# Performance work log

Measured on AMD Instinct MI355X. Metric: run time of the kernel, lower is better.

## Reference

```python
import jax, jax.numpy as jnp
import numpy as np

N_NODES = 50000
N_EDGES = 800000
IN_DIM = 128
HID_DIM = 256
OUT_DIM = 5
BATCH = 50000  # batch_size in module; view(batch_size, 5)


def _sage_conv(x, src, dst, Wl, bl, Wr):
    # PyG SAGEConv (aggr='mean', root_weight=True, normalize=False):
    #   out = lin_l(mean_{j in N(i)} x_j) + lin_r(x_i)
    msgs = x[src]                                            # [E, d]
    agg = jax.ops.segment_sum(msgs, dst, num_segments=N_NODES)
    cnt = jax.ops.segment_sum(jnp.ones((src.shape[0],), x.dtype), dst,
                              num_segments=N_NODES)          # [N]
    mean = agg / jnp.maximum(cnt, 1.0)[:, None]              # 0 for isolated nodes
    return mean @ Wl.T + bl + x @ Wr.T


def setup_inputs() -> dict:
    key = jax.random.key(0)
    ks = jax.random.split(key, 8)
    x = jax.random.normal(ks[0], (N_NODES, IN_DIM), dtype=jnp.float32)
    edge_index = jax.random.randint(ks[1], (2, N_EDGES), 0, N_NODES, dtype=jnp.int64)
    s1 = 1.0 / np.sqrt(IN_DIM)
    s2 = 1.0 / np.sqrt(HID_DIM)
    W1l = jax.random.uniform(ks[2], (HID_DIM, IN_DIM), jnp.float32, -s1, s1)
    b1l = jax.random.uniform(ks[3], (HID_DIM,), jnp.float32, -s1, s1)
    W1r = jax.random.uniform(ks[4], (HID_DIM, IN_DIM), jnp.float32, -s1, s1)
    W2l = jax.random.uniform(ks[5], (OUT_DIM, HID_DIM), jnp.float32, -s2, s2)
    b2l = jax.random.uniform(ks[6], (OUT_DIM,), jnp.float32, -s2, s2)
    W2r = jax.random.uniform(ks[7], (OUT_DIM, HID_DIM), jnp.float32, -s2, s2)
    return {"x": x, "edge_index": edge_index,
            "W1l": W1l, "b1l": b1l, "W1r": W1r,
            "W2l": W2l, "b2l": b2l, "W2r": W2r}


def reference(x, edge_index, W1l, b1l, W1r, W2l, b2l, W2r):
    src, dst = edge_index[0], edge_index[1]
    h = jax.nn.relu(_sage_conv(x, src, dst, W1l, b1l, W1r))   # [N, hidden]
    h = jax.nn.relu(_sage_conv(h, src, dst, W2l, b2l, W2r))   # [N, out]
    return h.reshape(BATCH, 5)
```

## Files before the change

### kernel.cpp

```cpp
#include <hip/hip_runtime.h>

static constexpr int NN = 50000;
static constexpr int NE = 800000;
static constexpr int D0 = 128;
static constexpr int D1 = 256;
static constexpr int D2 = 5;

static constexpr int XB = (NN * 32 + 255) / 256;
static constexpr int WB = (D1 * 64) / 256;
static constexpr int PB = 4;

static constexpr int BSZ   = 512;
static constexpr int NBUK  = (NN + BSZ - 1) / BSZ;
static constexpr int CAP   = 9216;
static constexpr int CB    = 400;
static constexpr int CHUNK = 2000;

using short8  = __attribute__((ext_vector_type(8))) short;
using floatx4 = __attribute__((ext_vector_type(4))) float;

__device__ __forceinline__ unsigned short f2b(float f) {
  union { float f; unsigned u; } v; v.f = f;
  unsigned r = v.u + 0x7fffu + ((v.u >> 16) & 1u);
  return (unsigned short)(r >> 16);
}
__device__ __forceinline__ float b2f(unsigned short s) {
  union { unsigned u; float f; } v; v.u = ((unsigned)s) << 16;
  return v.f;
}

__global__ __launch_bounds__(256) void k_prepA(
    const float* __restrict__ x, unsigned short* __restrict__ ab,
    const float* __restrict__ W1l, const float* __restrict__ W1r,
    unsigned short* __restrict__ wb, const float* __restrict__ W2l,
    const float* __restrict__ W2r, unsigned short* __restrict__ w2b,
    const int* __restrict__ src, const int* __restrict__ dst,
    int* __restrict__ gcur, uint2* __restrict__ slab) {
  __shared__ int hist[128], bstart[128], gbase[128], hcur[128], sscan[128];
  __shared__ uint2 pairs[CHUNK];
  const int b = blockIdx.x, t = threadIdx.x;
  if (b < XB) {
    int idx = b * 256 + t;
    if (idx < NN * 32) {
      int node = idx >> 5, cg = idx & 31;
      float4 v = *(const float4*)(x + (size_t)node * D0 + cg * 4);
      ushort4 o;
      o.x = f2b(v.x); o.y = f2b(v.y); o.z = f2b(v.z); o.w = f2b(v.w);
      *(ushort4*)(ab + (size_t)node * 256 + 128 + cg * 4) = o;
    }
    return;
  }
  if (b < XB + WB) {
    int idx = (b - XB) * 256 + t;
    int c = idx >> 6, k = (idx & 63) * 4;
    const float* srcp = (k < 128) ? (W1l + (size_t)c * 128 + k)
                                  : (W1r + (size_t)c * 128 + (k - 128));
    float4 v = *(const float4*)srcp;
    ushort4 o;
    o.x = f2b(v.x); o.y = f2b(v.y); o.z = f2b(v.z); o.w = f2b(v.w);
    *(ushort4*)(wb + (size_t)c * 256 + k) = o;
    return;
  }
  if (b < XB + WB + PB) {
    int idx = (b - XB - WB) * 256 + t;
    int n = idx >> 6, k = (idx & 63) * 4;
    float4 v = {0.f, 0.f, 0.f, 0.f};
    if (n < 5) v = *(const float4*)(W2l + (size_t)n * D1 + k);
    else if (n < 10) v = *(const float4*)(W2r + (size_t)(n - 5) * D1 + k);
    ushort4 o;
    o.x = f2b(v.x); o.y = f2b(v.y); o.z = f2b(v.z); o.w = f2b(v.w);
    *(ushort4*)(w2b + (size_t)n * 256 + k) = o;
    return;
  }
  const int ba = b - (XB + WB + PB);
  const int e0 = ba * CHUNK;
  if (t < 128) hist[t] = 0;
  __syncthreads();
  for (int j = t; j < CHUNK; j += 256)
    atomicAdd(&hist[dst[e0 + j] >> 9], 1);
  __syncthreads();
  if (t < 128) sscan[t] = hist[t];
  __syncthreads();
  for (int dd = 1; dd < 128; dd <<= 1) {
    int u = (t >= dd && t < 128) ? sscan[t - dd] : 0;
    __syncthreads();
    if (t < 128) sscan[t] += u;
    __syncthreads();
  }
  if (t < 128) {
    bstart[t] = sscan[t] - hist[t];
    gbase[t] = (t < NBUK && hist[t] > 0) ? atomicAdd(&gcur[t], hist[t]) : 0;
    hcur[t] = 0;
  }
  __syncthreads();
  for (int j = t; j < CHUNK; j += 256) {
    const int s = src[e0 + j], d = dst[e0 + j];
    const int bk = d >> 9;
    const int pos = bstart[bk] + atomicAdd(&hcur[bk], 1);
    pairs[pos] = make_uint2((unsigned)s, (unsigned)d);
  }
  __syncthreads();
  for (int j = t; j < CHUNK; j += 256) {
    const uint2 pr = pairs[j];
    const int bk = (int)pr.y >> 9;
    slab[(size_t)bk * CAP + gbase[bk] + (j - bstart[bk])] = pr;
  }
}

__global__ __launch_bounds__(512) void k_bucketBC(
    const uint2* __restrict__ slab, const int* __restrict__ gcur,
    int* __restrict__ cur, float* __restrict__ inv,
    int* __restrict__ esort) {
  __shared__ int cnt[BSZ], s[BSZ], lcur[BSZ], g[128];
  const int b = blockIdx.x, t = threadIdx.x;
  const int n0 = b << 9;
  cnt[t] = 0;
  if (t < 128) g[t] = (t < NBUK) ? gcur[t] : 0;
  __syncthreads();
  for (int dd = 1; dd < 128; dd <<= 1) {
    int u = (t >= dd && t < 128) ? g[t - dd] : 0;
    __syncthreads();
    if (t < 128) g[t] += u;
    __syncthreads();
  }
  const int bbase = (b == 0) ? 0 : g[b - 1];
  const int cntE = gcur[b];
  const uint2* sp = slab + (size_t)b * CAP;
  for (int j = t; j < cntE; j += 512)
    atomicAdd(&cnt[(int)sp[j].y - n0], 1);
  __syncthreads();
  s[t] = cnt[t];
  __syncthreads();
  for (int dd = 1; dd < BSZ; dd <<= 1) {
    int u = (t >= dd) ? s[t - dd] : 0;
    __syncthreads();
    s[t] += u;
    __syncthreads();
  }
  const int start = bbase + (s[t] - cnt[t]);
  const int node = n0 + t;
  if (node < NN) {
    cur[node] = start;
    inv[node] = 1.0f / (float)max(cnt[t], 1);
  }
  lcur[t] = start;
  if (b == NBUK - 1 && t == 0) cur[NN] = NE;
  __syncthreads();
  for (int j = t; j < cntE; j += 512) {
    const uint2 pr = sp[j];
    const int p = atomicAdd(&lcur[(int)pr.y - n0], 1);
    esort[p] = (int)pr.x;
  }
}

__global__ __launch_bounds__(256) void k_agg1(
    unsigned short* __restrict__ ab, const int* __restrict__ esort,
    const int* __restrict__ cur, const float* __restrict__ inv) {
  const int i = (blockIdx.x * 256 + threadIdx.x) >> 6;
  const int lane = threadIdx.x & 63;
  if (i >= NN) return;
  int e = cur[i];
  const int end = cur[i + 1];
  float a0 = 0.f, b0 = 0.f, a1 = 0.f, b1 = 0.f;
  float a2 = 0.f, b2 = 0.f, a3 = 0.f, b3 = 0.f;
  const unsigned short* xb = ab + 128 + lane * 2;
  while (e < end && (e & 3)) {
    const unsigned v = *(const unsigned*)(xb + (size_t)esort[e] * 256);
    a0 += b2f((unsigned short)v); b0 += b2f((unsigned short)(v >> 16));
    ++e;
  }
  for (; e + 7 < end; e += 8) {
    const int4 s0 = *(const int4*)(esort + e);
    const int4 s1 = *(const int4*)(esort + e + 4);
    const unsigned v0 = *(const unsigned*)(xb + (size_t)s0.x * 256);
    const unsigned v1 = *(const unsigned*)(xb + (size_t)s0.y * 256);
    const unsigned v2 = *(const unsigned*)(xb + (size_t)s0.z * 256);
    const unsigned v3 = *(const unsigned*)(xb + (size_t)s0.w * 256);
    const unsigned v4 = *(const unsigned*)(xb + (size_t)s1.x * 256);
    const unsigned v5 = *(const unsigned*)(xb + (size_t)s1.y * 256);
    const unsigned v6 = *(const unsigned*)(xb + (size_t)s1.z * 256);
    const unsigned v7 = *(const unsigned*)(xb + (size_t)s1.w * 256);
    a0 += b2f((unsigned short)v0); b0 += b2f((unsigned short)(v0 >> 16));
    a1 += b2f((unsigned short)v1); b1 += b2f((unsigned short)(v1 >> 16));
    a2 += b2f((unsigned short)v2); b2 += b2f((unsigned short)(v2 >> 16));
    a3 += b2f((unsigned short)v3); b3 += b2f((unsigned short)(v3 >> 16));
    a0 += b2f((unsigned short)v4); b0 += b2f((unsigned short)(v4 >> 16));
    a1 += b2f((unsigned short)v5); b1 += b2f((unsigned short)(v5 >> 16));
    a2 += b2f((unsigned short)v6); b2 += b2f((unsigned short)(v6 >> 16));
    a3 += b2f((unsigned short)v7); b3 += b2f((unsigned short)(v7 >> 16));
  }
  if (e + 3 < end) {
    const int4 s0 = *(const int4*)(esort + e);
    const unsigned v0 = *(const unsigned*)(xb + (size_t)s0.x * 256);
    const unsigned v1 = *(const unsigned*)(xb + (size_t)s0.y * 256);
    const unsigned v2 = *(const unsigned*)(xb + (size_t)s0.z * 256);
    const unsigned v3 = *(const unsigned*)(xb + (size_t)s0.w * 256);
    a0 += b2f((unsigned short)v0); b0 += b2f((unsigned short)(v0 >> 16));
    a1 += b2f((unsigned short)v1); b1 += b2f((unsigned short)(v1 >> 16));
    a2 += b2f((unsigned short)v2); b2 += b2f((unsigned short)(v2 >> 16));
    a3 += b2f((unsigned short)v3); b3 += b2f((unsigned short)(v3 >> 16));
    e += 4;
  }
  for (; e < end; ++e) {
    const unsigned v = *(const unsigned*)(xb + (size_t)esort[e] * 256);
    a0 += b2f((unsigned short)v); b0 += b2f((unsigned short)(v >> 16));
  }
  const float sc = inv[i];
  const float sa = (a0 + a1) + (a2 + a3);
  const float sb = (b0 + b1) + (b2 + b3);
  const unsigned out =
      ((unsigned)f2b(sb * sc) << 16) | (unsigned)f2b(sa * sc);
  *(unsigned*)(ab + (size_t)i * 256 + lane * 2) = out;
}

__global__ __launch_bounds__(256) void k_gemm1f(
    const unsigned short* __restrict__ ab, const unsigned short* __restrict__ wb,
    const unsigned short* __restrict__ w2b, const float* __restrict__ b1l,
    float* __restrict__ tt, float* __restrict__ rp) {
  __shared__ short sAB[2 * 128 * 72];
  short* sA = sAB;
  short* sB = sAB + 128 * 72;
  const int tid = threadIdx.x;
  const int row0 = blockIdx.y * 128;
  const int hf = blockIdx.x;
  const int col0 = hf * 128;
  const int wave = tid >> 6, lane = tid & 63;
  const int quad = lane >> 4, m16 = lane & 15;
  const int wm = wave & 1, wn = wave >> 1;
  const int lr = tid >> 2;
  const int lk = (tid & 3) * 8;

  floatx4 acc[4][4];
#pragma unroll
  for (int a = 0; a < 4; ++a)
#pragma unroll
    for (int b = 0; b < 4; ++b) acc[a][b] = {0.f, 0.f, 0.f, 0.f};

  const int gr0 = row0 + lr, gr1 = row0 + lr + 64;
  const bool ok0 = gr0 < NN, ok1 = gr1 < NN;
  const unsigned short* aptr0 = ab + (size_t)gr0 * 256 + lk;
  const unsigned short* aptr1 = ab + (size_t)gr1 * 256 + lk;
  const unsigned short* bptr0 = wb + (size_t)(col0 + lr) * 256 + lk;
  const unsigned short* bptr1 = wb + (size_t)(col0 + lr + 64) * 256 + lk;
  short* sA0 = &sA[lr * 72 + lk];
  short* sA1 = &sA[(lr + 64) * 72 + lk];
  short* sB0 = &sB[lr * 72 + lk];
  short* sB1 = &sB[(lr + 64) * 72 + lk];
  const uint4 zz = make_uint4(0, 0, 0, 0);

  for (int kk = 0; kk < 256; kk += 64) {
    const uint4 a00 = ok0 ? *(const uint4*)(aptr0 + kk) : zz;
    const uint4 a01 = ok0 ? *(const uint4*)(aptr0 + kk + 32) : zz;
    const uint4 a10 = ok1 ? *(const uint4*)(aptr1 + kk) : zz;
    const uint4 a11 = ok1 ? *(const uint4*)(aptr1 + kk + 32) : zz;
    const uint4 b00 = *(const uint4*)(bptr0 + kk);
    const uint4 b01 = *(const uint4*)(bptr0 + kk + 32);
    const uint4 b10 = *(const uint4*)(bptr1 + kk);
    const uint4 b11 = *(const uint4*)(bptr1 + kk + 32);
    __syncthreads();
    *(uint4*)sA0 = a00;
    *(uint4*)(sA0 + 32) = a01;
    *(uint4*)sA1 = a10;
    *(uint4*)(sA1 + 32) = a11;
    *(uint4*)sB0 = b00;
    *(uint4*)(sB0 + 32) = b01;
    *(uint4*)sB1 = b10;
    *(uint4*)(sB1 + 32) = b11;
    __syncthreads();
#pragma unroll
    for (int ko = 0; ko < 64; ko += 32) {
      short8 af[4], bf[4];
#pragma unroll
      for (int mt = 0; mt < 4; ++mt)
        af[mt] =
            *(const short8*)&sA[(wm * 64 + mt * 16 + m16) * 72 + ko + quad * 8];
#pragma unroll
      for (int nt = 0; nt < 4; ++nt)
        bf[nt] =
            *(const short8*)&sB[(wn * 64 + nt * 16 + m16) * 72 + ko + quad * 8];
#pragma unroll
      for (int mt = 0; mt < 4; ++mt)
#pragma unroll
        for (int nt = 0; nt < 4; ++nt)
          acc[mt][nt] = __builtin_amdgcn_mfma_f32_16x16x32_bf16(
              af[mt], bf[nt], acc[mt][nt], 0, 0, 0);
    }
  }

  __syncthreads();
  short* sH = sAB;
#pragma unroll
  for (int nt = 0; nt < 4; ++nt) {
    const int cl = wn * 64 + nt * 16 + m16;
    const float bias = b1l[col0 + cl];
#pragma unroll
    for (int mt = 0; mt < 4; ++mt)
#pragma unroll
      for (int rg = 0; rg < 4; ++rg) {
        const int rl = wm * 64 + mt * 16 + quad * 4 + rg;
        sH[rl * 136 + cl] = (short)f2b(fmaxf(acc[mt][nt][rg] + bias, 0.f));
      }
  }
  __syncthreads();
  floatx4 c2[2] = {{0.f, 0.f, 0.f, 0.f}, {0.f, 0.f, 0.f, 0.f}};
#pragma unroll
  for (int kb = 0; kb < 4; ++kb) {
    const short8 bf2 =
        *(const short8*)&w2b[m16 * 256 + col0 + kb * 32 + quad * 8];
#pragma unroll
    for (int i = 0; i < 2; ++i) {
      const int mrow = (wave * 2 + i) * 16 + m16;
      const short8 af2 = *(const short8*)&sH[mrow * 136 + kb * 32 + quad * 8];
      c2[i] = __builtin_amdgcn_mfma_f32_16x16x32_bf16(af2, bf2, c2[i], 0, 0, 0);
    }
  }
#pragma unroll
  for (int i = 0; i < 2; ++i) {
    const int rbase = row0 + (wave * 2 + i) * 16 + quad * 4;
#pragma unroll
    for (int rg = 0; rg < 4; ++rg) {
      const int row = rbase + rg;
      if (row < NN) {
        if (m16 < 5)
          tt[(size_t)row * 16 + hf * 8 + m16] = c2[i][rg];
        else if (m16 < 10)
          rp[(size_t)hf * ((size_t)NN * 8) + (size_t)row * 8 + (m16 - 5)] =
              c2[i][rg];
      }
    }
  }
}

__global__ __launch_bounds__(256) void k_layer2(
    const float* __restrict__ tt, const float* __restrict__ rp,
    const int* __restrict__ esort, const int* __restrict__ cur,
    const float* __restrict__ inv, const float* __restrict__ b2l,
    float* __restrict__ out) {
  const int node = blockIdx.x * 16 + (threadIdx.x >> 4);
  const int l = threadIdx.x & 15;
  if (node >= NN) return;
  const int beg = cur[node], end = cur[node + 1];
  float s0 = 0.f, s1 = 0.f, s2 = 0.f, s3 = 0.f, s4 = 0.f;
  for (int e = beg + l; e < end; e += 16) {
    const float* tp = tt + (size_t)esort[e] * 16;
    const float4 p0 = *(const float4*)tp;
    const float q0 = tp[4];
    const float4 p1 = *(const float4*)(tp + 8);
    const float q1 = tp[12];
    s0 += p0.x + p1.x;
    s1 += p0.y + p1.y;
    s2 += p0.z + p1.z;
    s3 += p0.w + p1.w;
    s4 += q0 + q1;
  }
#pragma unroll
  for (int m = 1; m < 16; m <<= 1) {
    s0 += __shfl_xor(s0, m, 64);
    s1 += __shfl_xor(s1, m, 64);
    s2 += __shfl_xor(s2, m, 64);
    s3 += __shfl_xor(s3, m, 64);
    s4 += __shfl_xor(s4, m, 64);
  }
  if (l == 0) {
    const float sc = inv[node];
    const float* r0 = rp + (size_t)node * 8;
    const float* r1 = rp + (size_t)NN * 8 + (size_t)node * 8;
    out[(size_t)node * D2 + 0] = fmaxf(s0 * sc + b2l[0] + r0[0] + r1[0], 0.f);
    out[(size_t)node * D2 + 1] = fmaxf(s1 * sc + b2l[1] + r0[1] + r1[1], 0.f);
    out[(size_t)node * D2 + 2] = fmaxf(s2 * sc + b2l[2] + r0[2] + r1[2], 0.f);
    out[(size_t)node * D2 + 3] = fmaxf(s3 * sc + b2l[3] + r0[3] + r1[3], 0.f);
    out[(size_t)node * D2 + 4] = fmaxf(s4 * sc + b2l[4] + r0[4] + r1[4], 0.f);
  }
}

extern "C" void kernel_launch(void* const* d_in, const int* in_sizes, int n_in,
                              void* d_out, int out_size, void* d_ws,
                              size_t ws_size, hipStream_t stream) {
  const float* x   = (const float*)d_in[0];
  const int*   ei  = (const int*)d_in[1];
  const int*   src = ei;
  const int*   dst = ei + NE;
  const float* W1l = (const float*)d_in[2];
  const float* b1l = (const float*)d_in[3];
  const float* W1r = (const float*)d_in[4];
  const float* W2l = (const float*)d_in[5];
  const float* b2l = (const float*)d_in[6];
  const float* W2r = (const float*)d_in[7];
  float* out = (float*)d_out;

  unsigned short* ab  = (unsigned short*)d_ws;
  unsigned short* wb  = ab + (size_t)NN * 256;
  unsigned short* w2b = wb + 256 * 256;
  float* tt   = (float*)(w2b + 16 * 256);
  float* rp   = tt + (size_t)NN * 16;
  uint2* slab = (uint2*)(rp + (size_t)NN * 16);
  int*   gcur = (int*)(slab + (size_t)NBUK * CAP);
  int*   cur  = gcur + 128;
  int*   esort = cur + NN + 1;
  float* inv  = (float*)(esort + NE);

  hipMemsetAsync(gcur, 0, 128 * sizeof(int), stream);

  k_prepA<<<XB + WB + PB + CB, 256, 0, stream>>>(x, ab, W1l, W1r, wb, W2l, W2r,
                                                 w2b, src, dst, gcur, slab);
  k_bucketBC<<<NBUK, 512, 0, stream>>>(slab, gcur, cur, inv, esort);
  k_agg1<<<(NN * 64 + 255) / 256, 256, 0, stream>>>(ab, esort, cur, inv);
  dim3 g1(2, (NN + 127) / 128);
  k_gemm1f<<<g1, 256, 0, stream>>>(ab, wb, w2b, b1l, tt, rp);
  k_layer2<<<(NN + 15) / 16, 256, 0, stream>>>(tt, rp, esort, cur, inv, b2l,
                                               out);
}
```

Baseline: 182.8 us.

## Fuse all stages into one persistent kernel with software grid barriers

Replaces five separate kernel launches with a single persistent kernel of 512 blocks that runs the conversion, bucketing, CSR build, aggregation, GEMM and layer-2 stages in sequence, separated by atomic-counter grid barriers. Destination buckets shrink from 512 to 256 nodes, with a matching smaller slab capacity. The aim is to remove launch gaps and tail effects between stages. In exchange each stage runs with a fixed grid, and the spin barriers depend on all 512 blocks being co-resident, which is not guaranteed under a normal launch and could deadlock or hit the guard timeout.

```diff
diff --git a/kernel.cpp b/kernel.cpp
--- a/kernel.cpp
+++ b/kernel.cpp
@@ -6,15 +6,18 @@
 static constexpr int D1 = 256;
 static constexpr int D2 = 5;
 
-static constexpr int XB = (NN * 32 + 255) / 256;
-static constexpr int WB = (D1 * 64) / 256;
-static constexpr int PB = 4;
-
-static constexpr int BSZ   = 512;
+static constexpr int NB  = 512;
+static constexpr int TPB = 256;
+
+static constexpr int BSZ   = 256;
 static constexpr int NBUK  = (NN + BSZ - 1) / BSZ;
-static constexpr int CAP   = 9216;
+static constexpr int CAP   = 4800;
 static constexpr int CB    = 400;
 static constexpr int CHUNK = 2000;
+
+static constexpr int NTILE = 2 * ((NN + 127) / 128);
+
+static constexpr int SMEM_BYTES = 36864;
 
 using short8  = __attribute__((ext_vector_type(8))) short;
 using floatx4 = __attribute__((ext_vector_type(4))) float;
@@ -29,347 +32,360 @@
   return v.f;
 }
 
-__global__ __launch_bounds__(256) void k_prepA(
-    const float* __restrict__ x, unsigned short* __restrict__ ab,
-    const float* __restrict__ W1l, const float* __restrict__ W1r,
-    unsigned short* __restrict__ wb, const float* __restrict__ W2l,
-    const float* __restrict__ W2r, unsigned short* __restrict__ w2b,
-    const int* __restrict__ src, const int* __restrict__ dst,
-    int* __restrict__ gcur, uint2* __restrict__ slab) {
-  __shared__ int hist[128], bstart[128], gbase[128], hcur[128], sscan[128];
-  __shared__ uint2 pairs[CHUNK];
-  const int b = blockIdx.x, t = threadIdx.x;
-  if (b < XB) {
-    int idx = b * 256 + t;
-    if (idx < NN * 32) {
-      int node = idx >> 5, cg = idx & 31;
-      float4 v = *(const float4*)(x + (size_t)node * D0 + cg * 4);
-      ushort4 o;
-      o.x = f2b(v.x); o.y = f2b(v.y); o.z = f2b(v.z); o.w = f2b(v.w);
-      *(ushort4*)(ab + (size_t)node * 256 + 128 + cg * 4) = o;
-    }
-    return;
-  }
-  if (b < XB + WB) {
-    int idx = (b - XB) * 256 + t;
-    int c = idx >> 6, k = (idx & 63) * 4;
+__device__ __forceinline__ void gbar(int* ctr) {
+  __syncthreads();
+  if (threadIdx.x == 0) {
+    __threadfence();
+    atomicAdd(ctr, 1);
+    long guard = 0;
+    while (__hip_atomic_load(ctr, __ATOMIC_ACQUIRE, __HIP_MEMORY_SCOPE_AGENT) <
+               NB &&
+           ++guard < 100000000L) {
+    }
+  }
+  __syncthreads();
+}
+
+__global__ __launch_bounds__(256, 2) void k_all(
+    const float* __restrict__ x, const int* __restrict__ src,
+    const int* __restrict__ dst, const float* __restrict__ W1l,
+    const float* __restrict__ b1l, const float* __restrict__ W1r,
+    const float* __restrict__ W2l, const float* __restrict__ b2l,
+    const float* __restrict__ W2r, unsigned short* __restrict__ ab,
+    unsigned short* __restrict__ wb, unsigned short* __restrict__ w2b,
+    float* __restrict__ tt, float* __restrict__ rp, uint2* __restrict__ slab,
+    int* __restrict__ gcur, int* __restrict__ cur, float* __restrict__ inv,
+    int* __restrict__ esort, int* __restrict__ ctr, float* __restrict__ out) {
+  __shared__ __align__(16) char smem[SMEM_BYTES];
+  const int t = threadIdx.x;
+  const int bx = blockIdx.x;
+  const int gid = bx * TPB + t;
+
+  for (int idx = gid; idx < NN * 32; idx += NB * TPB) {
+    const int node = idx >> 5, cg4 = idx & 31;
+    const float4 v = *(const float4*)(x + (size_t)node * D0 + cg4 * 4);
+    ushort4 o;
+    o.x = f2b(v.x); o.y = f2b(v.y); o.z = f2b(v.z); o.w = f2b(v.w);
+    *(ushort4*)(ab + (size_t)node * 256 + 128 + cg4 * 4) = o;
+  }
+  for (int idx = gid; idx < 256 * 64; idx += NB * TPB) {
+    const int c = idx >> 6, k = (idx & 63) * 4;
     const float* srcp = (k < 128) ? (W1l + (size_t)c * 128 + k)
                                   : (W1r + (size_t)c * 128 + (k - 128));
-    float4 v = *(const float4*)srcp;
+    const float4 v = *(const float4*)srcp;
     ushort4 o;
     o.x = f2b(v.x); o.y = f2b(v.y); o.z = f2b(v.z); o.w = f2b(v.w);
     *(ushort4*)(wb + (size_t)c * 256 + k) = o;
-    return;
-  }
-  if (b < XB + WB + PB) {
-    int idx = (b - XB - WB) * 256 + t;
-    int n = idx >> 6, k = (idx & 63) * 4;
+  }
+  if (gid < 1024) {
+    const int n = gid >> 6, k = (gid & 63) * 4;
     float4 v = {0.f, 0.f, 0.f, 0.f};
     if (n < 5) v = *(const float4*)(W2l + (size_t)n * D1 + k);
     else if (n < 10) v = *(const float4*)(W2r + (size_t)(n - 5) * D1 + k);
     ushort4 o;
     o.x = f2b(v.x); o.y = f2b(v.y); o.z = f2b(v.z); o.w = f2b(v.w);
     *(ushort4*)(w2b + (size_t)n * 256 + k) = o;
-    return;
-  }
-  const int ba = b - (XB + WB + PB);
-  const int e0 = ba * CHUNK;
-  if (t < 128) hist[t] = 0;
-  __syncthreads();
-  for (int j = t; j < CHUNK; j += 256)
-    atomicAdd(&hist[dst[e0 + j] >> 9], 1);
-  __syncthreads();
-  if (t < 128) sscan[t] = hist[t];
-  __syncthreads();
-  for (int dd = 1; dd < 128; dd <<= 1) {
-    int u = (t >= dd && t < 128) ? sscan[t - dd] : 0;
-    __syncthreads();
-    if (t < 128) sscan[t] += u;
-    __syncthreads();
-  }
-  if (t < 128) {
-    bstart[t] = sscan[t] - hist[t];
+  }
+
+  if (bx < CB) {
+    int* hist = (int*)smem;
+    int* ss = hist + 256;
+    int* bstart = ss + 256;
+    int* hcur = bstart + 256;
+    int* gbase = hcur + 256;
+    uint2* pairs = (uint2*)(gbase + 256);
+    const int e0 = bx * CHUNK;
+    hist[t] = 0;
+    __syncthreads();
+    for (int j = t; j < CHUNK; j += TPB) atomicAdd(&hist[dst[e0 + j] >> 8], 1);
+    __syncthreads();
+    ss[t] = hist[t];
+    __syncthreads();
+    for (int dd = 1; dd < 256; dd <<= 1) {
+      const int u = (t >= dd) ? ss[t - dd] : 0;
+      __syncthreads();
+      ss[t] += u;
+      __syncthreads();
+    }
+    bstart[t] = ss[t] - hist[t];
+    hcur[t] = 0;
     gbase[t] = (t < NBUK && hist[t] > 0) ? atomicAdd(&gcur[t], hist[t]) : 0;
-    hcur[t] = 0;
-  }
-  __syncthreads();
-  for (int j = t; j < CHUNK; j += 256) {
-    const int s = src[e0 + j], d = dst[e0 + j];
-    const int bk = d >> 9;
-    const int pos = bstart[bk] + atomicAdd(&hcur[bk], 1);
-    pairs[pos] = make_uint2((unsigned)s, (unsigned)d);
-  }
-  __syncthreads();
-  for (int j = t; j < CHUNK; j += 256) {
-    const uint2 pr = pairs[j];
-    const int bk = (int)pr.y >> 9;
-    slab[(size_t)bk * CAP + gbase[bk] + (j - bstart[bk])] = pr;
-  }
-}
-
-__global__ __launch_bounds__(512) void k_bucketBC(
-    const uint2* __restrict__ slab, const int* __restrict__ gcur,
-    int* __restrict__ cur, float* __restrict__ inv,
-    int* __restrict__ esort) {
-  __shared__ int cnt[BSZ], s[BSZ], lcur[BSZ], g[128];
-  const int b = blockIdx.x, t = threadIdx.x;
-  const int n0 = b << 9;
-  cnt[t] = 0;
-  if (t < 128) g[t] = (t < NBUK) ? gcur[t] : 0;
-  __syncthreads();
-  for (int dd = 1; dd < 128; dd <<= 1) {
-    int u = (t >= dd && t < 128) ? g[t - dd] : 0;
-    __syncthreads();
-    if (t < 128) g[t] += u;
-    __syncthreads();
-  }
-  const int bbase = (b == 0) ? 0 : g[b - 1];
-  const int cntE = gcur[b];
-  const uint2* sp = slab + (size_t)b * CAP;
-  for (int j = t; j < cntE; j += 512)
-    atomicAdd(&cnt[(int)sp[j].y - n0], 1);
-  __syncthreads();
-  s[t] = cnt[t];
-  __syncthreads();
-  for (int dd = 1; dd < BSZ; dd <<= 1) {
-    int u = (t >= dd) ? s[t - dd] : 0;
-    __syncthreads();
-    s[t] += u;
-    __syncthreads();
-  }
-  const int start = bbase + (s[t] - cnt[t]);
-  const int node = n0 + t;
-  if (node < NN) {
-    cur[node] = start;
-    inv[node] = 1.0f / (float)max(cnt[t], 1);
-  }
-  lcur[t] = start;
-  if (b == NBUK - 1 && t == 0) cur[NN] = NE;
-  __syncthreads();
-  for (int j = t; j < cntE; j += 512) {
-    const uint2 pr = sp[j];
-    const int p = atomicAdd(&lcur[(int)pr.y - n0], 1);
-    esort[p] = (int)pr.x;
-  }
-}
-
-__global__ __launch_bounds__(256) void k_agg1(
-    unsigned short* __restrict__ ab, const int* __restrict__ esort,
-    const int* __restrict__ cur, const float* __restrict__ inv) {
-  const int i = (blockIdx.x * 256 + threadIdx.x) >> 6;
-  const int lane = threadIdx.x & 63;
-  if (i >= NN) return;
-  int e = cur[i];
-  const int end = cur[i + 1];
-  float a0 = 0.f, b0 = 0.f, a1 = 0.f, b1 = 0.f;
-  float a2 = 0.f, b2 = 0.f, a3 = 0.f, b3 = 0.f;
-  const unsigned short* xb = ab + 128 + lane * 2;
-  while (e < end && (e & 3)) {
-    const unsigned v = *(const unsigned*)(xb + (size_t)esort[e] * 256);
-    a0 += b2f((unsigned short)v); b0 += b2f((unsigned short)(v >> 16));
-    ++e;
-  }
-  for (; e + 7 < end; e += 8) {
-    const int4 s0 = *(const int4*)(esort + e);
-    const int4 s1 = *(const int4*)(esort + e + 4);
-    const unsigned v0 = *(const unsigned*)(xb + (size_t)s0.x * 256);
-    const unsigned v1 = *(const unsigned*)(xb + (size_t)s0.y * 256);
-    const unsigned v2 = *(const unsigned*)(xb + (size_t)s0.z * 256);
-    const unsigned v3 = *(const unsigned*)(xb + (size_t)s0.w * 256);
-    const unsigned v4 = *(const unsigned*)(xb + (size_t)s1.x * 256);
-    const unsigned v5 = *(const unsigned*)(xb + (size_t)s1.y * 256);
-    const unsigned v6 = *(const unsigned*)(xb + (size_t)s1.z * 256);
-    const unsigned v7 = *(const unsigned*)(xb + (size_t)s1.w * 256);
-    a0 += b2f((unsigned short)v0); b0 += b2f((unsigned short)(v0 >> 16));
-    a1 += b2f((unsigned short)v1); b1 += b2f((unsigned short)(v1 >> 16));
-    a2 += b2f((unsigned short)v2); b2 += b2f((unsigned short)(v2 >> 16));
-    a3 += b2f((unsigned short)v3); b3 += b2f((unsigned short)(v3 >> 16));
-    a0 += b2f((unsigned short)v4); b0 += b2f((unsigned short)(v4 >> 16));
-    a1 += b2f((unsigned short)v5); b1 += b2f((unsigned short)(v5 >> 16));
-    a2 += b2f((unsigned short)v6); b2 += b2f((unsigned short)(v6 >> 16));
-    a3 += b2f((unsigned short)v7); b3 += b2f((unsigned short)(v7 >> 16));
-  }
-  if (e + 3 < end) {
-    const int4 s0 = *(const int4*)(esort + e);
-    const unsigned v0 = *(const unsigned*)(xb + (size_t)s0.x * 256);
-    const unsigned v1 = *(const unsigned*)(xb + (size_t)s0.y * 256);
-    const unsigned v2 = *(const unsigned*)(xb + (size_t)s0.z * 256);
-    const unsigned v3 = *(const unsigned*)(xb + (size_t)s0.w * 256);
-    a0 += b2f((unsigned short)v0); b0 += b2f((unsigned short)(v0 >> 16));
-    a1 += b2f((unsigned short)v1); b1 += b2f((unsigned short)(v1 >> 16));
-    a2 += b2f((unsigned short)v2); b2 += b2f((unsigned short)(v2 >> 16));
-    a3 += b2f((unsigned short)v3); b3 += b2f((unsigned short)(v3 >> 16));
-    e += 4;
-  }
-  for (; e < end; ++e) {
-    const unsigned v = *(const unsigned*)(xb + (size_t)esort[e] * 256);
-    a0 += b2f((unsigned short)v); b0 += b2f((unsigned short)(v >> 16));
-  }
-  const float sc = inv[i];
-  const float sa = (a0 + a1) + (a2 + a3);
-  const float sb = (b0 + b1) + (b2 + b3);
-  const unsigned out =
-      ((unsigned)f2b(sb * sc) << 16) | (unsigned)f2b(sa * sc);
-  *(unsigned*)(ab + (size_t)i * 256 + lane * 2) = out;
-}
-
-__global__ __launch_bounds__(256) void k_gemm1f(
-    const unsigned short* __restrict__ ab, const unsigned short* __restrict__ wb,
-    const unsigned short* __restrict__ w2b, const float* __restrict__ b1l,
-    float* __restrict__ tt, float* __restrict__ rp) {
-  __shared__ short sAB[2 * 128 * 72];
-  short* sA = sAB;
-  short* sB = sAB + 128 * 72;
-  const int tid = threadIdx.x;
-  const int row0 = blockIdx.y * 128;
-  const int hf = blockIdx.x;
-  const int col0 = hf * 128;
-  const int wave = tid >> 6, lane = tid & 63;
-  const int quad = lane >> 4, m16 = lane & 15;
-  const int wm = wave & 1, wn = wave >> 1;
-  const int lr = tid >> 2;
-  const int lk = (tid & 3) * 8;
-
-  floatx4 acc[4][4];
-#pragma unroll
-  for (int a = 0; a < 4; ++a)
-#pragma unroll
-    for (int b = 0; b < 4; ++b) acc[a][b] = {0.f, 0.f, 0.f, 0.f};
-
-  const int gr0 = row0 + lr, gr1 = row0 + lr + 64;
-  const bool ok0 = gr0 < NN, ok1 = gr1 < NN;
-  const unsigned short* aptr0 = ab + (size_t)gr0 * 256 + lk;
-  const unsigned short* aptr1 = ab + (size_t)gr1 * 256 + lk;
-  const unsigned short* bptr0 = wb + (size_t)(col0 + lr) * 256 + lk;
-  const unsigned short* bptr1 = wb + (size_t)(col0 + lr + 64) * 256 + lk;
-  short* sA0 = &sA[lr * 72 + lk];
-  short* sA1 = &sA[(lr + 64) * 72 + lk];
-  short* sB0 = &sB[lr * 72 + lk];
-  short* sB1 = &sB[(lr + 64) * 72 + lk];
-  const uint4 zz = make_uint4(0, 0, 0, 0);
-
-  for (int kk = 0; kk < 256; kk += 64) {
-    const uint4 a00 = ok0 ? *(const uint4*)(aptr0 + kk) : zz;
-    const uint4 a01 = ok0 ? *(const uint4*)(aptr0 + kk + 32) : zz;
-    const uint4 a10 = ok1 ? *(const uint4*)(aptr1 + kk) : zz;
-    const uint4 a11 = ok1 ? *(const uint4*)(aptr1 + kk + 32) : zz;
-    const uint4 b00 = *(const uint4*)(bptr0 + kk);
-    const uint4 b01 = *(const uint4*)(bptr0 + kk + 32);
-    const uint4 b10 = *(const uint4*)(bptr1 + kk);
-    const uint4 b11 = *(const uint4*)(bptr1 + kk + 32);
-    __syncthreads();
-    *(uint4*)sA0 = a00;
-    *(uint4*)(sA0 + 32) = a01;
-    *(uint4*)sA1 = a10;
-    *(uint4*)(sA1 + 32) = a11;
-    *(uint4*)sB0 = b00;
-    *(uint4*)(sB0 + 32) = b01;
-    *(uint4*)sB1 = b10;
-    *(uint4*)(sB1 + 32) = b11;
-    __syncthreads();
-#pragma unroll
-    for (int ko = 0; ko < 64; ko += 32) {
-      short8 af[4], bf[4];
-#pragma unroll
-      for (int mt = 0; mt < 4; ++mt)
-        af[mt] =
-            *(const short8*)&sA[(wm * 64 + mt * 16 + m16) * 72 + ko + quad * 8];
-#pragma unroll
-      for (int nt = 0; nt < 4; ++nt)
-        bf[nt] =
-            *(const short8*)&sB[(wn * 64 + nt * 16 + m16) * 72 + ko + quad * 8];
-#pragma unroll
-      for (int mt = 0; mt < 4; ++mt)
-#pragma unroll
-        for (int nt = 0; nt < 4; ++nt)
-          acc[mt][nt] = __builtin_amdgcn_mfma_f32_16x16x32_bf16(
-              af[mt], bf[nt], acc[mt][nt], 0, 0, 0);
-    }
-  }
-
-  __syncthreads();
-  short* sH = sAB;
-#pragma unroll
-  for (int nt = 0; nt < 4; ++nt) {
-    const int cl = wn * 64 + nt * 16 + m16;
-    const float bias = b1l[col0 + cl];
-#pragma unroll
-    for (int mt = 0; mt < 4; ++mt)
-#pragma unroll
-      for (int rg = 0; rg < 4; ++rg) {
-        const int rl = wm * 64 + mt * 16 + quad * 4 + rg;
-        sH[rl * 136 + cl] = (short)f2b(fmaxf(acc[mt][nt][rg] + bias, 0.f));
-      }
-  }
-  __syncthreads();
-  floatx4 c2[2] = {{0.f, 0.f, 0.f, 0.f}, {0.f, 0.f, 0.f, 0.f}};
-#pragma unroll
-  for (int kb = 0; kb < 4; ++kb) {
-    const short8 bf2 =
-        *(const short8*)&w2b[m16 * 256 + col0 + kb * 32 + quad * 8];
-#pragma unroll
-    for (int i = 0; i < 2; ++i) {
-      const int mrow = (wave * 2 + i) * 16 + m16;
-      const short8 af2 = *(const short8*)&sH[mrow * 136 + kb * 32 + quad * 8];
-      c2[i] = __builtin_amdgcn_mfma_f32_16x16x32_bf16(af2, bf2, c2[i], 0, 0, 0);
-    }
-  }
-#pragma unroll
-  for (int i = 0; i < 2; ++i) {
-    const int rbase = row0 + (wave * 2 + i) * 16 + quad * 4;
-#pragma unroll
-    for (int rg = 0; rg < 4; ++rg) {
-      const int row = rbase + rg;
-      if (row < NN) {
-        if (m16 < 5)
-          tt[(size_t)row * 16 + hf * 8 + m16] = c2[i][rg];
-        else if (m16 < 10)
-          rp[(size_t)hf * ((size_t)NN * 8) + (size_t)row * 8 + (m16 - 5)] =
-              c2[i][rg];
-      }
-    }
-  }
-}
-
-__global__ __launch_bounds__(256) void k_layer2(
-    const float* __restrict__ tt, const float* __restrict__ rp,
-    const int* __restrict__ esort, const int* __restrict__ cur,
-    const float* __restrict__ inv, const float* __restrict__ b2l,
-    float* __restrict__ out) {
-  const int node = blockIdx.x * 16 + (threadIdx.x >> 4);
-  const int l = threadIdx.x & 15;
-  if (node >= NN) return;
-  const int beg = cur[node], end = cur[node + 1];
-  float s0 = 0.f, s1 = 0.f, s2 = 0.f, s3 = 0.f, s4 = 0.f;
-  for (int e = beg + l; e < end; e += 16) {
-    const float* tp = tt + (size_t)esort[e] * 16;
-    const float4 p0 = *(const float4*)tp;
-    const float q0 = tp[4];
-    const float4 p1 = *(const float4*)(tp + 8);
-    const float q1 = tp[12];
-    s0 += p0.x + p1.x;
-    s1 += p0.y + p1.y;
-    s2 += p0.z + p1.z;
-    s3 += p0.w + p1.w;
-    s4 += q0 + q1;
-  }
-#pragma unroll
-  for (int m = 1; m < 16; m <<= 1) {
-    s0 += __shfl_xor(s0, m, 64);
-    s1 += __shfl_xor(s1, m, 64);
-    s2 += __shfl_xor(s2, m, 64);
-    s3 += __shfl_xor(s3, m, 64);
-    s4 += __shfl_xor(s4, m, 64);
-  }
-  if (l == 0) {
-    const float sc = inv[node];
-    const float* r0 = rp + (size_t)node * 8;
-    const float* r1 = rp + (size_t)NN * 8 + (size_t)node * 8;
-    out[(size_t)node * D2 + 0] = fmaxf(s0 * sc + b2l[0] + r0[0] + r1[0], 0.f);
-    out[(size_t)node * D2 + 1] = fmaxf(s1 * sc + b2l[1] + r0[1] + r1[1], 0.f);
-    out[(size_t)node * D2 + 2] = fmaxf(s2 * sc + b2l[2] + r0[2] + r1[2], 0.f);
-    out[(size_t)node * D2 + 3] = fmaxf(s3 * sc + b2l[3] + r0[3] + r1[3], 0.f);
-    out[(size_t)node * D2 + 4] = fmaxf(s4 * sc + b2l[4] + r0[4] + r1[4], 0.f);
+    __syncthreads();
+    for (int j = t; j < CHUNK; j += TPB) {
+      const int s = src[e0 + j], d = dst[e0 + j];
+      const int bk = d >> 8;
+      const int pos = bstart[bk] + atomicAdd(&hcur[bk], 1);
+      pairs[pos] = make_uint2((unsigned)s, (unsigned)d);
+    }
+    __syncthreads();
+    for (int j = t; j < CHUNK; j += TPB) {
+      const uint2 pr = pairs[j];
+      const int bk = (int)pr.y >> 8;
+      slab[(size_t)bk * CAP + gbase[bk] + (j - bstart[bk])] = pr;
+    }
+  }
+  gbar(ctr + 0);
+
+  if (bx < NBUK) {
+    int* bs = (int*)smem;
+    int* cnt = bs + 256;
+    int* s = cnt + 256;
+    int* lcur = s + 256;
+    const int n0 = bx << 8;
+    bs[t] = (t < NBUK) ? gcur[t] : 0;
+    cnt[t] = 0;
+    __syncthreads();
+    for (int dd = 1; dd < 256; dd <<= 1) {
+      const int u = (t >= dd) ? bs[t - dd] : 0;
+      __syncthreads();
+      bs[t] += u;
+      __syncthreads();
+    }
+    const int bbase = (bx == 0) ? 0 : bs[bx - 1];
+    const int cntE = gcur[bx];
+    const uint2* sp = slab + (size_t)bx * CAP;
+    for (int j = t; j < cntE; j += TPB) atomicAdd(&cnt[(int)sp[j].y & 255], 1);
+    __syncthreads();
+    s[t] = cnt[t];
+    __syncthreads();
+    for (int dd = 1; dd < 256; dd <<= 1) {
+      const int u = (t >= dd) ? s[t - dd] : 0;
+      __syncthreads();
+      s[t] += u;
+      __syncthreads();
+    }
+    const int start = bbase + (s[t] - cnt[t]);
+    const int node = n0 + t;
+    if (node < NN) {
+      cur[node] = start;
+      inv[node] = 1.0f / (float)max(cnt[t], 1);
+    }
+    lcur[t] = start;
+    if (bx == 0 && t == 0) cur[NN] = bs[NBUK - 1];
+    __syncthreads();
+    for (int j = t; j < cntE; j += TPB) {
+      const uint2 pr = sp[j];
+      const int p = atomicAdd(&lcur[(int)pr.y & 255], 1);
+      esort[p] = (int)pr.x;
+    }
+  }
+  gbar(ctr + 1);
+
+  {
+    const int lane = t & 63;
+    const unsigned short* xb = ab + 128 + lane * 2;
+    for (int i = gid >> 6; i < NN; i += (NB * TPB) >> 6) {
+      int e = cur[i];
+      const int end = cur[i + 1];
+      float a0 = 0.f, b0 = 0.f, a1 = 0.f, b1 = 0.f;
+      float a2 = 0.f, b2 = 0.f, a3 = 0.f, b3 = 0.f;
+      while (e < end && (e & 3)) {
+        const unsigned v = *(const unsigned*)(xb + (size_t)esort[e] * 256);
+        a0 += b2f((unsigned short)v); b0 += b2f((unsigned short)(v >> 16));
+        ++e;
+      }
+      for (; e + 7 < end; e += 8) {
+        const int4 s0 = *(const int4*)(esort + e);
+        const int4 s1 = *(const int4*)(esort + e + 4);
+        const unsigned v0 = *(const unsigned*)(xb + (size_t)s0.x * 256);
+        const unsigned v1 = *(const unsigned*)(xb + (size_t)s0.y * 256);
+        const unsigned v2 = *(const unsigned*)(xb + (size_t)s0.z * 256);
+        const unsigned v3 = *(const unsigned*)(xb + (size_t)s0.w * 256);
+        const unsigned v4 = *(const unsigned*)(xb + (size_t)s1.x * 256);
+        const unsigned v5 = *(const unsigned*)(xb + (size_t)s1.y * 256);
+        const unsigned v6 = *(const unsigned*)(xb + (size_t)s1.z * 256);
+        const unsigned v7 = *(const unsigned*)(xb + (size_t)s1.w * 256);
+        a0 += b2f((unsigned short)v0); b0 += b2f((unsigned short)(v0 >> 16));
+        a1 += b2f((unsigned short)v1); b1 += b2f((unsigned short)(v1 >> 16));
+        a2 += b2f((unsigned short)v2); b2 += b2f((unsigned short)(v2 >> 16));
+        a3 += b2f((unsigned short)v3); b3 += b2f((unsigned short)(v3 >> 16));
+        a0 += b2f((unsigned short)v4); b0 += b2f((unsigned short)(v4 >> 16));
+        a1 += b2f((unsigned short)v5); b1 += b2f((unsigned short)(v5 >> 16));
+        a2 += b2f((unsigned short)v6); b2 += b2f((unsigned short)(v6 >> 16));
+        a3 += b2f((unsigned short)v7); b3 += b2f((unsigned short)(v7 >> 16));
+      }
+      if (e + 3 < end) {
+        const int4 s0 = *(const int4*)(esort + e);
+        const unsigned v0 = *(const unsigned*)(xb + (size_t)s0.x * 256);
+        const unsigned v1 = *(const unsigned*)(xb + (size_t)s0.y * 256);
+        const unsigned v2 = *(const unsigned*)(xb + (size_t)s0.z * 256);
+        const unsigned v3 = *(const unsigned*)(xb + (size_t)s0.w * 256);
+        a0 += b2f((unsigned short)v0); b0 += b2f((unsigned short)(v0 >> 16));
+        a1 += b2f((unsigned short)v1); b1 += b2f((unsigned short)(v1 >> 16));
+        a2 += b2f((unsigned short)v2); b2 += b2f((unsigned short)(v2 >> 16));
+        a3 += b2f((unsigned short)v3); b3 += b2f((unsigned short)(v3 >> 16));
+        e += 4;
+      }
+      for (; e < end; ++e) {
+        const unsigned v = *(const unsigned*)(xb + (size_t)esort[e] * 256);
+        a0 += b2f((unsigned short)v); b0 += b2f((unsigned short)(v >> 16));
+      }
+      const float sc = inv[i];
+      const float sa = (a0 + a1) + (a2 + a3);
+      const float sb = (b0 + b1) + (b2 + b3);
+      const unsigned o =
+          ((unsigned)f2b(sb * sc) << 16) | (unsigned)f2b(sa * sc);
+      *(unsigned*)(ab + (size_t)i * 256 + lane * 2) = o;
+    }
+  }
+  gbar(ctr + 2);
+
+  {
+    short* sA = (short*)smem;
+    short* sB = sA + 128 * 72;
+    const int wave = t >> 6, lane = t & 63;
+    const int quad = lane >> 4, m16 = lane & 15;
+    const int wm = wave & 1, wn = wave >> 1;
+    const int lr = t >> 2;
+    const int lk = (t & 3) * 8;
+    const uint4 zz = make_uint4(0, 0, 0, 0);
+    for (int tile = bx; tile < NTILE; tile += NB) {
+      const int row0 = (tile >> 1) * 128;
+      const int hf = tile & 1;
+      const int col0 = hf * 128;
+      floatx4 acc[4][4];
+#pragma unroll
+      for (int a = 0; a < 4; ++a)
+#pragma unroll
+        for (int b = 0; b < 4; ++b) acc[a][b] = {0.f, 0.f, 0.f, 0.f};
+      const int gr0 = row0 + lr, gr1 = row0 + lr + 64;
+      const bool ok0 = gr0 < NN, ok1 = gr1 < NN;
+      const unsigned short* aptr0 = ab + (size_t)gr0 * 256 + lk;
+      const unsigned short* aptr1 = ab + (size_t)gr1 * 256 + lk;
+      const unsigned short* bptr0 = wb + (size_t)(col0 + lr) * 256 + lk;
+      const unsigned short* bptr1 = wb + (size_t)(col0 + lr + 64) * 256 + lk;
+      short* sA0 = &sA[lr * 72 + lk];
+      short* sA1 = &sA[(lr + 64) * 72 + lk];
+      short* sB0 = &sB[lr * 72 + lk];
+      short* sB1 = &sB[(lr + 64) * 72 + lk];
+      for (int kk = 0; kk < 256; kk += 64) {
+        const uint4 a00 = ok0 ? *(const uint4*)(aptr0 + kk) : zz;
+        const uint4 a01 = ok0 ? *(const uint4*)(aptr0 + kk + 32) : zz;
+        const uint4 a10 = ok1 ? *(const uint4*)(aptr1 + kk) : zz;
+        const uint4 a11 = ok1 ? *(const uint4*)(aptr1 + kk + 32) : zz;
+        const uint4 b00 = *(const uint4*)(bptr0 + kk);
+        const uint4 b01 = *(const uint4*)(bptr0 + kk + 32);
+        const uint4 b10 = *(const uint4*)(bptr1 + kk);
+        const uint4 b11 = *(const uint4*)(bptr1 + kk + 32);
+        __syncthreads();
+        *(uint4*)sA0 = a00;
+        *(uint4*)(sA0 + 32) = a01;
+        *(uint4*)sA1 = a10;
+        *(uint4*)(sA1 + 32) = a11;
+        *(uint4*)sB0 = b00;
+        *(uint4*)(sB0 + 32) = b01;
+        *(uint4*)sB1 = b10;
+        *(uint4*)(sB1 + 32) = b11;
+        __syncthreads();
+#pragma unroll
+        for (int ko = 0; ko < 64; ko += 32) {
+          short8 af[4], bf[4];
+#pragma unroll
+          for (int mt = 0; mt < 4; ++mt)
+            af[mt] = *(const short8*)&sA[(wm * 64 + mt * 16 + m16) * 72 + ko +
+                                         quad * 8];
+#pragma unroll
+          for (int nt = 0; nt < 4; ++nt)
+            bf[nt] = *(const short8*)&sB[(wn * 64 + nt * 16 + m16) * 72 + ko +
+                                         quad * 8];
+#pragma unroll
+          for (int mt = 0; mt < 4; ++mt)
+#pragma unroll
+            for (int nt = 0; nt < 4; ++nt)
+              acc[mt][nt] = __builtin_amdgcn_mfma_f32_16x16x32_bf16(
+                  af[mt], bf[nt], acc[mt][nt], 0, 0, 0);
+        }
+      }
+      __syncthreads();
+      short* sH = (short*)smem;
+#pragma unroll
+      for (int nt = 0; nt < 4; ++nt) {
+        const int cl = wn * 64 + nt * 16 + m16;
+        const float bias = b1l[col0 + cl];
+#pragma unroll
+        for (int mt = 0; mt < 4; ++mt)
+#pragma unroll
+          for (int rg = 0; rg < 4; ++rg) {
+            const int rl = wm * 64 + mt * 16 + quad * 4 + rg;
+            sH[rl * 136 + cl] = (short)f2b(fmaxf(acc[mt][nt][rg] + bias, 0.f));
+          }
+      }
+      __syncthreads();
+      floatx4 c2[2] = {{0.f, 0.f, 0.f, 0.f}, {0.f, 0.f, 0.f, 0.f}};
+#pragma unroll
+      for (int kb = 0; kb < 4; ++kb) {
+        const short8 bf2 =
+            *(const short8*)&w2b[m16 * 256 + col0 + kb * 32 + quad * 8];
+#pragma unroll
+        for (int i = 0; i < 2; ++i) {
+          const int mrow = (wave * 2 + i) * 16 + m16;
+          const short8 af2 =
+              *(const short8*)&sH[mrow * 136 + kb * 32 + quad * 8];
+          c2[i] =
+              __builtin_amdgcn_mfma_f32_16x16x32_bf16(af2, bf2, c2[i], 0, 0, 0);
+        }
+      }
+#pragma unroll
+      for (int i = 0; i < 2; ++i) {
+        const int rbase = row0 + (wave * 2 + i) * 16 + quad * 4;
+#pragma unroll
+        for (int rg = 0; rg < 4; ++rg) {
+          const int row = rbase + rg;
+          if (row < NN) {
+            if (m16 < 5)
+              tt[(size_t)row * 16 + hf * 8 + m16] = c2[i][rg];
+            else if (m16 < 10)
+              rp[(size_t)hf * ((size_t)NN * 8) + (size_t)row * 8 + (m16 - 5)] =
+                  c2[i][rg];
+          }
+        }
+      }
+      __syncthreads();
+    }
+  }
+  gbar(ctr + 3);
+
+  {
+    const int l = t & 15;
+    for (int node = bx * 16 + (t >> 4); node < NN; node += NB * 16) {
+      const int beg = cur[node], end = cur[node + 1];
+      float s0 = 0.f, s1 = 0.f, s2 = 0.f, s3 = 0.f, s4 = 0.f;
+      for (int e = beg + l; e < end; e += 16) {
+        const float* tp = tt + (size_t)esort[e] * 16;
+        const float4 p0 = *(const float4*)tp;
+        const float q0 = tp[4];
+        const float4 p1 = *(const float4*)(tp + 8);
+        const float q1 = tp[12];
+        s0 += p0.x + p1.x;
+        s1 += p0.y + p1.y;
+        s2 += p0.z + p1.z;
+        s3 += p0.w + p1.w;
+        s4 += q0 + q1;
+      }
+#pragma unroll
+      for (int m = 1; m < 16; m <<= 1) {
+        s0 += __shfl_xor(s0, m, 64);
+        s1 += __shfl_xor(s1, m, 64);
+        s2 += __shfl_xor(s2, m, 64);
+        s3 += __shfl_xor(s3, m, 64);
+        s4 += __shfl_xor(s4, m, 64);
+      }
+      if (l == 0) {
+        const float sc = inv[node];
+        const float* r0 = rp + (size_t)node * 8;
+        const float* r1 = rp + (size_t)NN * 8 + (size_t)node * 8;
+        out[(size_t)node * D2 + 0] =
+            fmaxf(s0 * sc + b2l[0] + r0[0] + r1[0], 0.f);
+        out[(size_t)node * D2 + 1] =
+            fmaxf(s1 * sc + b2l[1] + r0[1] + r1[1], 0.f);
+        out[(size_t)node * D2 + 2] =
+            fmaxf(s2 * sc + b2l[2] + r0[2] + r1[2], 0.f);
+        out[(size_t)node * D2 + 3] =
+            fmaxf(s3 * sc + b2l[3] + r0[3] + r1[3], 0.f);
+        out[(size_t)node * D2 + 4] =
+            fmaxf(s4 * sc + b2l[4] + r0[4] + r1[4], 0.f);
+      }
+    }
   }
 }
 
@@ -388,25 +404,28 @@
   const float* W2r = (const float*)d_in[7];
   float* out = (float*)d_out;
 
-  unsigned short* ab  = (unsigned short*)d_ws;
+  int*   ctr  = (int*)d_ws;
+  int*   gcur = ctr + 8;
+  unsigned short* ab  = (unsigned short*)(gcur + 248);
   unsigned short* wb  = ab + (size_t)NN * 256;
   unsigned short* w2b = wb + 256 * 256;
-  float* tt   = (float*)(w2b + 16 * 256);
+  uint2* slab = (uint2*)(w2b + 16 * 256);
+  float* tt   = (float*)(slab + (size_t)NBUK * CAP);
   float* rp   = tt + (size_t)NN * 16;
-  uint2* slab = (uint2*)(rp + (size_t)NN * 16);
-  int*   gcur = (int*)(slab + (size_t)NBUK * CAP);
-  int*   cur  = gcur + 128;
+  int*   cur  = (int*)(rp + (size_t)NN * 16);
   int*   esort = cur + NN + 1;
   float* inv  = (float*)(esort + NE);
 
-  hipMemsetAsync(gcur, 0, 128 * sizeof(int), stream);
-
-  k_prepA<<<XB + WB + PB + CB, 256, 0, stream>>>(x, ab, W1l, W1r, wb, W2l, W2r,
-                                                 w2b, src, dst, gcur, slab);
-  k_bucketBC<<<NBUK, 512, 0, stream>>>(slab, gcur, cur, inv, esort);
-  k_agg1<<<(NN * 64 + 255) / 256, 256, 0, stream>>>(ab, esort, cur, inv);
-  dim3 g1(2, (NN + 127) / 128);
-  k_gemm1f<<<g1, 256, 0, stream>>>(ab, wb, w2b, b1l, tt, rp);
-  k_layer2<<<(NN + 15) / 16, 256, 0, stream>>>(tt, rp, esort, cur, inv, b2l,
-                                               out);
+  hipMemsetAsync(ctr, 0, 256 * sizeof(int), stream);
+
+  void* kargs[] = {(void*)&x,    (void*)&src, (void*)&dst,  (void*)&W1l,
+                   (void*)&b1l,  (void*)&W1r, (void*)&W2l,  (void*)&b2l,
+                   (void*)&W2r,  (void*)&ab,  (void*)&wb,   (void*)&w2b,
+                   (void*)&tt,   (void*)&rp,  (void*)&slab, (void*)&gcur,
+                   (void*)&cur,  (void*)&inv, (void*)&esort, (void*)&ctr,
+                   (void*)&out};
+  (void)kargs;
+  k_all<<<NB, TPB, 0, stream>>>(x, src, dst, W1l, b1l, W1r, W2l, b2l, W2r, ab,
+                                wb, w2b, tt, rp, slab, gcur, cur, inv, esort,
+                                ctr, out);
 }
```

Result: slower. 601.2 us (+228.8%).
